# Kernel tuning notes

Hardware: AMD Instinct MI355X
Metric: run time of the kernel (lower is better)

Reference implementation:

```python
import jax, jax.numpy as jnp
import numpy as np

B, CENT, IN_CH, OUT_CH, NDIAG = 32, 2, 8, 16, 64


def setup_inputs() -> dict:
    key = jax.random.key(0)
    k1, k2, k3 = jax.random.split(key, 3)
    D = jax.random.normal(k1, (B, CENT, IN_CH, NDIAG), dtype=jnp.float32)
    C = jax.random.normal(k2, (CENT, IN_CH, NDIAG, NDIAG), dtype=jnp.float32)
    # weight is constrained non-negative (NonNeg constraint + tf.abs in build)
    w = jax.random.uniform(k3, (NDIAG, CENT, IN_CH, OUT_CH), dtype=jnp.float32)
    return {"D": D, "C": C, "w": w}


def reference(D, C, w):
    # Faithful math: u from SVD of C (s, v unused in the original call);
    # spd = sum_{c,n} u @ diag(einsum('bcnd,dcno', D, w)) @ u^T
    w = jnp.abs(w)  # mirrors tf.abs(self.w) in build
    u, _, _ = jnp.linalg.svd(C, full_matrices=False)  # (c, n, d, d)
    svec = jnp.einsum('bcnd,dcno->bcnod', D, w)        # diagonal entries, no diag() blow-up
    # u diag(svec) u^T, fused: avoids materializing (b,c,n,o,d,d) diag matrix
    spd = jnp.einsum('cnid,bcnod,cnjd->boij', u, svec, u)  # (b, o, d, d)
    return spd
```

## Files before the change

kernel.cpp:

```cpp
#include <hip/hip_runtime.h>
#include <math.h>


#define NSWEEP 8
#define NROUND (NSWEEP * 63)

__device__ __forceinline__ float bper(int paddr, float v) {
    return __int_as_float(__builtin_amdgcn_ds_bpermute(paddr, __float_as_int(v)));
}

__device__ __forceinline__ float pdot16(const float (&a)[16], const float (&b)[16]) {
    float d0 = 0.f, d1 = 0.f, d2 = 0.f, d3 = 0.f;
    #pragma unroll
    for (int i = 0; i < 16; i += 4) {
        d0 = fmaf(a[i],     b[i],     d0);
        d1 = fmaf(a[i + 1], b[i + 1], d1);
        d2 = fmaf(a[i + 2], b[i + 2], d2);
        d3 = fmaf(a[i + 3], b[i + 3], d3);
    }
    return (d0 + d1) + (d2 + d3);
}

__global__ __launch_bounds__(256, 1) void eig_kernel(const float* __restrict__ C,
                                                     float* __restrict__ ut) {
    __shared__ float pex[4][64];
    __shared__ float sn[64];

    const int mat  = blockIdx.x;
    const int tid  = threadIdx.x;
    const int wv   = tid >> 6;
    const int lane = tid & 63;
    const int row0 = wv << 4;
    const float* Cm = C + mat * 4096;

    float g[16];
    #pragma unroll
    for (int i = 0; i < 16; i++) g[i] = Cm[(row0 + i) * 64 + lane];

    float nrm;
    {
        pex[wv][lane] = pdot16(g, g);
        __syncthreads();
        nrm = (pex[0][lane] + pex[1][lane]) + (pex[2][lane] + pex[3][lane]);
        __syncthreads();
    }

    int m = 1;
    for (int r = 0; r < NROUND; ++r) {
        const int partner = lane ^ m;
        const int paddr   = partner << 2;

        float tmp[16];
        #pragma unroll
        for (int i = 0; i < 16; i++) tmp[i] = bper(paddr, g[i]);
        const float pn = bper(paddr, nrm);

        const float part = pdot16(g, tmp);
        pex[wv][lane] = part;
        __syncthreads();
        const float gam = (pex[0][lane] + pex[1][lane]) + (pex[2][lane] + pex[3][lane]);
        __syncthreads();

        const bool  is_p = lane < partner;
        const float diff = pn - nrm;
        const float num  = is_p ? diff : -diff;
        const float zeta = num * 0.5f * __builtin_amdgcn_rcpf(gam);
        const float t0   = copysignf(1.f, zeta) *
                           __builtin_amdgcn_rcpf(fabsf(zeta) + sqrtf(fmaf(zeta, zeta, 1.f)));
        const float t    = (fabsf(gam) > 1e-30f) ? t0 : 0.f;
        const float c    = __builtin_amdgcn_rsqf(fmaf(t, t, 1.f));
        const float s    = t * c;
        const float sa   = is_p ? -s : s;
        const float ta   = is_p ? -t : t;

        #pragma unroll
        for (int i = 0; i < 16; i++) g[i] = fmaf(c, g[i], sa * tmp[i]);
        nrm = fmaf(ta, gam, nrm);

        m = (m == 63) ? 1 : m + 1;
    }

    {
        const float part = pdot16(g, g);
        pex[wv][lane] = part;
        __syncthreads();
        nrm = (pex[0][lane] + pex[1][lane]) + (pex[2][lane] + pex[3][lane]);
    }

    if (wv == 0) sn[lane] = nrm;
    __syncthreads();
    int rank = 0;
    #pragma unroll 8
    for (int e = 0; e < 64; e++) {
        const float ne = sn[e];
        rank += (ne > nrm) || (ne == nrm && e < lane);
    }

    const float inv = __builtin_amdgcn_rsqf(fmaxf(nrm, 1e-30f));
    float* dst = ut + (mat * 64 + rank) * 64 + row0;
    #pragma unroll
    for (int i = 0; i < 16; i++) dst[i] = g[i] * inv;
}

__global__ __launch_bounds__(256) void spd_kernel(const float* __restrict__ D,
                                                  const float* __restrict__ w,
                                                  const float* __restrict__ ut,
                                                  float* __restrict__ out) {
    __shared__ __align__(16) float U[64][64];
    __shared__ float t[64];

    const int bid = blockIdx.x;
    const int b = bid >> 4, o = bid & 15;
    const int tid = threadIdx.x;
    const int ti = tid & 15, tj = tid >> 4;

    float acc[4][4] = {{0.f, 0.f, 0.f, 0.f}, {0.f, 0.f, 0.f, 0.f},
                       {0.f, 0.f, 0.f, 0.f}, {0.f, 0.f, 0.f, 0.f}};

    for (int cn = 0; cn < 16; cn++) {
        __syncthreads();
        const float4* src = (const float4*)(ut + cn * 4096);
        float4* dstU = (float4*)(&U[0][0]);
        #pragma unroll
        for (int idx = tid; idx < 1024; idx += 256) dstU[idx] = src[idx];
        if (tid < 64) {
            int d = tid;
            float dv = D[(b * 16 + cn) * 64 + d];
            float wv = fabsf(w[(d * 16 + cn) * 16 + o]);
            t[d] = dv * wv;
        }
        __syncthreads();

        #pragma unroll 4
        for (int d = 0; d < 64; d++) {
            float td = t[d];
            float4 uiv = *(const float4*)(&U[d][ti * 4]);
            float4 ujv = *(const float4*)(&U[d][tj * 4]);
            float si0 = td * uiv.x, si1 = td * uiv.y, si2 = td * uiv.z, si3 = td * uiv.w;
            acc[0][0] += si0 * ujv.x; acc[0][1] += si0 * ujv.y; acc[0][2] += si0 * ujv.z; acc[0][3] += si0 * ujv.w;
            acc[1][0] += si1 * ujv.x; acc[1][1] += si1 * ujv.y; acc[1][2] += si1 * ujv.z; acc[1][3] += si1 * ujv.w;
            acc[2][0] += si2 * ujv.x; acc[2][1] += si2 * ujv.y; acc[2][2] += si2 * ujv.z; acc[2][3] += si2 * ujv.w;
            acc[3][0] += si3 * ujv.x; acc[3][1] += si3 * ujv.y; acc[3][2] += si3 * ujv.z; acc[3][3] += si3 * ujv.w;
        }
    }

    float* obase = out + (size_t)bid * 4096;
    #pragma unroll
    for (int k = 0; k < 4; k++) {
        float4 v = make_float4(acc[k][0], acc[k][1], acc[k][2], acc[k][3]);
        *(float4*)(&obase[(ti * 4 + k) * 64 + tj * 4]) = v;
    }
}

extern "C" void kernel_launch(void* const* d_in, const int* in_sizes, int n_in,
                              void* d_out, int out_size, void* d_ws, size_t ws_size,
                              hipStream_t stream) {
    const float* D = (const float*)d_in[0];
    const float* C = (const float*)d_in[1];
    const float* w = (const float*)d_in[2];
    float* out = (float*)d_out;
    float* ut  = (float*)d_ws;

    hipLaunchKernelGGL(eig_kernel, dim3(16), dim3(256), 0, stream, C, ut);
    hipLaunchKernelGGL(spd_kernel, dim3(512), dim3(256), 0, stream, D, w, ut, out);
}
```

Measured before the change: 319.6 us.

## Split spd reduction dim across waves with 8x8 register tiles and LDS reduce

The spd kernel now has each wave handle a quarter of the diagonal dimension. Each lane accumulates an 8x8 output tile instead of 4x4, which cuts shared-memory reads per FMA. Partial sums from the four waves are combined through a 32KB shared buffer in two chunks, then written out. This raises register and LDS use and adds extra barriers and a reduction step.

```diff
diff --git a/kernel.cpp b/kernel.cpp
--- a/kernel.cpp
+++ b/kernel.cpp
@@ -107,48 +107,78 @@
                                                   const float* __restrict__ ut,
                                                   float* __restrict__ out) {
     __shared__ __align__(16) float U[64][64];
-    __shared__ float t[64];
+    __shared__ float ts[64];
+    __shared__ float red[4][32][64];
 
-    const int bid = blockIdx.x;
-    const int b = bid >> 4, o = bid & 15;
-    const int tid = threadIdx.x;
-    const int ti = tid & 15, tj = tid >> 4;
+    const int bid  = blockIdx.x;
+    const int b    = bid >> 4, o = bid & 15;
+    const int tid  = threadIdx.x;
+    const int wv   = tid >> 6;
+    const int lane = tid & 63;
+    const int ti   = lane & 7, tj = lane >> 3;
+    const int d0   = wv << 4;
 
-    float acc[4][4] = {{0.f, 0.f, 0.f, 0.f}, {0.f, 0.f, 0.f, 0.f},
-                       {0.f, 0.f, 0.f, 0.f}, {0.f, 0.f, 0.f, 0.f}};
+    float acc[8][8];
+    #pragma unroll
+    for (int r = 0; r < 8; r++)
+        #pragma unroll
+        for (int c = 0; c < 8; c++) acc[r][c] = 0.f;
 
     for (int cn = 0; cn < 16; cn++) {
         __syncthreads();
         const float4* src = (const float4*)(ut + cn * 4096);
-        float4* dstU = (float4*)(&U[0][0]);
+        float4* dU = (float4*)(&U[0][0]);
         #pragma unroll
-        for (int idx = tid; idx < 1024; idx += 256) dstU[idx] = src[idx];
+        for (int k = 0; k < 4; k++) dU[tid + k * 256] = src[tid + k * 256];
         if (tid < 64) {
-            int d = tid;
-            float dv = D[(b * 16 + cn) * 64 + d];
-            float wv = fabsf(w[(d * 16 + cn) * 16 + o]);
-            t[d] = dv * wv;
+            const int d = tid;
+            const float dv = D[(b * 16 + cn) * 64 + d];
+            const float wva = fabsf(w[(d * 16 + cn) * 16 + o]);
+            ts[d] = dv * wva;
         }
         __syncthreads();
 
         #pragma unroll 4
-        for (int d = 0; d < 64; d++) {
-            float td = t[d];
-            float4 uiv = *(const float4*)(&U[d][ti * 4]);
-            float4 ujv = *(const float4*)(&U[d][tj * 4]);
-            float si0 = td * uiv.x, si1 = td * uiv.y, si2 = td * uiv.z, si3 = td * uiv.w;
-            acc[0][0] += si0 * ujv.x; acc[0][1] += si0 * ujv.y; acc[0][2] += si0 * ujv.z; acc[0][3] += si0 * ujv.w;
-            acc[1][0] += si1 * ujv.x; acc[1][1] += si1 * ujv.y; acc[1][2] += si1 * ujv.z; acc[1][3] += si1 * ujv.w;
-            acc[2][0] += si2 * ujv.x; acc[2][1] += si2 * ujv.y; acc[2][2] += si2 * ujv.z; acc[2][3] += si2 * ujv.w;
-            acc[3][0] += si3 * ujv.x; acc[3][1] += si3 * ujv.y; acc[3][2] += si3 * ujv.z; acc[3][3] += si3 * ujv.w;
+        for (int dd = 0; dd < 16; dd++) {
+            const int d = d0 + dd;
+            const float td = ts[d];
+            const float4* row = (const float4*)(&U[d][0]);
+            const float4 a0 = row[ti * 2], a1 = row[ti * 2 + 1];
+            const float4 b0 = row[tj * 2], b1 = row[tj * 2 + 1];
+            const float si[8] = {td * a0.x, td * a0.y, td * a0.z, td * a0.w,
+                                 td * a1.x, td * a1.y, td * a1.z, td * a1.w};
+            const float bb[8] = {b0.x, b0.y, b0.z, b0.w, b1.x, b1.y, b1.z, b1.w};
+            #pragma unroll
+            for (int r = 0; r < 8; r++)
+                #pragma unroll
+                for (int c = 0; c < 8; c++) acc[r][c] = fmaf(si[r], bb[c], acc[r][c]);
         }
     }
 
-    float* obase = out + (size_t)bid * 4096;
-    #pragma unroll
-    for (int k = 0; k < 4; k++) {
-        float4 v = make_float4(acc[k][0], acc[k][1], acc[k][2], acc[k][3]);
-        *(float4*)(&obase[(ti * 4 + k) * 64 + tj * 4]) = v;
+    float* ob = out + (size_t)bid * 4096;
+    for (int chunk = 0; chunk < 2; chunk++) {
+        __syncthreads();
+        #pragma unroll
+        for (int rr = 0; rr < 4; rr++)
+            #pragma unroll
+            for (int c = 0; c < 8; c++)
+                red[wv][rr * 8 + c][lane] = acc[chunk * 4 + rr][c];
+        __syncthreads();
+        #pragma unroll
+        for (int e = 0; e < 8; e++) {
+            const int f   = tid * 8 + e;
+            const int lf  = f >> 5;
+            const int loc = f & 31;
+            const float v = (red[0][loc][lf] + red[1][loc][lf]) +
+                            (red[2][loc][lf] + red[3][loc][lf]);
+            const int c_  = f & 7;
+            const int rr_ = (f >> 3) & 3;
+            const int ti_ = (f >> 5) & 7;
+            const int tj_ = f >> 8;
+            const int i   = ti_ * 8 + chunk * 4 + rr_;
+            const int j   = tj_ * 8 + c_;
+            ob[i * 64 + j] = v;
+        }
     }
 }
 
```

Measured after the change: 303.3 us. 5.1% less time.
